# Kernel optimization log

Measured on AMD Instinct MI355X. Metric: run time of the kernel, lower is better.

## Reference

```python
import jax, jax.numpy as jnp
import numpy as np

L_LAYERS = 2
N = 128
T = 64
K_BANDS = 30
KMOD = K_BANDS + 2  # 32
B = 4
G4 = 4 * N
EPS = 1e-5


def setup_inputs() -> dict:
    key = jax.random.key(0)
    ks = iter(jax.random.split(key, 32))
    s = 1.0 / np.sqrt(N)

    def u(shape):
        return jax.random.uniform(next(ks), shape, jnp.float32, -s, s)

    inp = {"x": jax.random.normal(next(ks), (B, KMOD, T, N), jnp.float32)}
    # temporal modules: KMOD LSTM/fc instances per layer
    inp["tw_ih"] = u((L_LAYERS, KMOD, 2, G4, N))
    inp["tw_hh"] = u((L_LAYERS, KMOD, 2, G4, N))
    inp["tb_ih"] = u((L_LAYERS, KMOD, 2, G4))
    inp["tb_hh"] = u((L_LAYERS, KMOD, 2, G4))
    inp["tfc_w"] = u((L_LAYERS, KMOD, N, 2 * N))
    inp["tfc_b"] = u((L_LAYERS, KMOD, N))
    inp["tgn_g"] = jnp.ones((L_LAYERS, N), jnp.float32)
    inp["tgn_b"] = jnp.zeros((L_LAYERS, N), jnp.float32)
    # band modules: T LSTM/fc instances per layer
    inp["bw_ih"] = u((L_LAYERS, T, 2, G4, N))
    inp["bw_hh"] = u((L_LAYERS, T, 2, G4, N))
    inp["bb_ih"] = u((L_LAYERS, T, 2, G4))
    inp["bb_hh"] = u((L_LAYERS, T, 2, G4))
    inp["bfc_w"] = u((L_LAYERS, T, N, 2 * N))
    inp["bfc_b"] = u((L_LAYERS, T, N))
    inp["bgn_g"] = jnp.ones((L_LAYERS, N), jnp.float32)
    inp["bgn_b"] = jnp.zeros((L_LAYERS, N), jnp.float32)
    return inp


def groupnorm(X, gamma, beta):
    # GroupNorm(1, N) on [B, N, K, T] == normalize over all non-batch dims,
    # per-channel affine on the last (N) dim of the [B, K, T, N] layout.
    mu = X.mean(axis=(1, 2, 3), keepdims=True)
    var = X.var(axis=(1, 2, 3), keepdims=True)
    return (X - mu) * jax.lax.rsqrt(var + EPS) * gamma + beta


def bilstm(x, w_ih, w_hh, b_ih, b_hh):
    # x: [B, S, N]; w_ih/w_hh: [2, 4N, N]; biases: [2, 4N]. PyTorch gate order i,f,g,o.
    Bb, S, n = x.shape

    def run(xs, wih, whh, b):
        pre = jnp.einsum('bsn,gn->bsg', xs, wih) + b  # [B, S, 4N]

        def step(carry, p):
            h, c = carry
            g = p + h @ whh.T
            i, f, gg, o = jnp.split(g, 4, axis=-1)
            c = jax.nn.sigmoid(f) * c + jax.nn.sigmoid(i) * jnp.tanh(gg)
            h = jax.nn.sigmoid(o) * jnp.tanh(c)
            return (h, c), h

        z = jnp.zeros((Bb, n), xs.dtype)
        _, hs = jax.lax.scan(step, (z, z), jnp.swapaxes(pre, 0, 1))
        return jnp.swapaxes(hs, 0, 1)  # [B, S, N]

    fwd = run(x, w_ih[0], w_hh[0], b_ih[0] + b_hh[0])
    bwd = run(x[:, ::-1], w_ih[1], w_hh[1], b_ih[1] + b_hh[1])[:, ::-1]
    return jnp.concatenate([fwd, bwd], axis=-1)  # [B, S, 2N]


# vmap over the per-instance (band or frame) leading axis of inputs and weights
vbilstm = jax.vmap(bilstm, in_axes=(0, 0, 0, 0, 0))


def temporal_module(X, w_ih, w_hh, b_ih, b_hh, fc_w, fc_b, g, b):
    skip = X  # [B, K, T, N]
    Xn = groupnorm(X, g, b)
    xs = jnp.swapaxes(Xn, 0, 1)  # [K, B, T, N]
    h = vbilstm(xs, w_ih, w_hh, b_ih, b_hh)  # [K, B, T, 2N]
    out = jnp.einsum('kbtd,knd->kbtn', h, fc_w) + fc_b[:, None, None, :]
    return jnp.swapaxes(out, 0, 1) + skip


def band_module(X, w_ih, w_hh, b_ih, b_hh, fc_w, fc_b, g, b):
    skip = X  # [B, K, T, N]
    Xn = groupnorm(X, g, b)
    xs = jnp.transpose(Xn, (2, 0, 1, 3))  # [T, B, K, N]
    h = vbilstm(xs, w_ih, w_hh, b_ih, b_hh)  # [T, B, K, 2N]
    out = jnp.einsum('tbkd,tnd->tbkn', h, fc_w) + fc_b[:, None, None, :]
    return jnp.transpose(out, (1, 2, 0, 3)) + skip


def reference(x, tw_ih, tw_hh, tb_ih, tb_hh, tfc_w, tfc_b, tgn_g, tgn_b,
              bw_ih, bw_hh, bb_ih, bb_hh, bfc_w, bfc_b, bgn_g, bgn_b):
    X = x
    for i in range(L_LAYERS):
        X = temporal_module(X, tw_ih[i], tw_hh[i], tb_ih[i], tb_hh[i],
                            tfc_w[i], tfc_b[i], tgn_g[i], tgn_b[i])
        X = band_module(X, bw_ih[i], bw_hh[i], bb_ih[i], bb_hh[i],
                        bfc_w[i], bfc_b[i], bgn_g[i], bgn_b[i])
    return X[:, :K_BANDS, :, :]
```

## Files before the change

kernel.cpp:

```cpp
#include <hip/hip_runtime.h>
#include <hip/hip_bf16.h>
#include <cstddef>

#define BB 4
#define KK 32
#define TTT 64
#define NNC 128
#define GG4 512

__device__ __forceinline__ float sigm(float x) { return 1.f / (1.f + __expf(-x)); }
__device__ __forceinline__ float tanh_fast(float x) {
    x = fminf(fmaxf(x, -15.f), 15.f);
    float e = __expf(2.f * x);
    return (e - 1.f) / (e + 1.f);
}

__global__ void k_copy_red(const float4* __restrict__ src, float4* __restrict__ dst,
                           float* __restrict__ red2) {
    const int i = blockIdx.x * 256 + threadIdx.x;
    const float4 v = src[i];
    dst[i] = v;
    float s  = v.x + v.y + v.z + v.w;
    float ss = v.x * v.x + v.y * v.y + v.z * v.z + v.w * v.w;
    for (int off = 32; off; off >>= 1) {
        s  += __shfl_down(s, off);
        ss += __shfl_down(ss, off);
    }
    __shared__ float l0[4], l1[4];
    const int w = threadIdx.x >> 6;
    if ((threadIdx.x & 63) == 0) { l0[w] = s; l1[w] = ss; }
    __syncthreads();
    if (threadIdx.x == 0) {
        const int b = blockIdx.x >> 8, slot = blockIdx.x & 255;
        red2[(b * 256 + slot) * 2]     = l0[0] + l0[1] + l0[2] + l0[3];
        red2[(b * 256 + slot) * 2 + 1] = l1[0] + l1[1] + l1[2] + l1[3];
    }
}

template <bool BAND>
__global__ __launch_bounds__(1024, 1) void k_pre(
    const float* __restrict__ X, float* __restrict__ pre,
    const float* __restrict__ red2,
    const float* __restrict__ w_ih,
    const float* __restrict__ b_ih, const float* __restrict__ b_hh,
    const float* __restrict__ gn_g, const float* __restrict__ gn_b,
    int layer)
{
    constexpr int S    = BAND ? 32 : 64;
    constexpr int INST = BAND ? 64 : 32;
    const int tid = threadIdx.x;
    const int g   = tid & 511;
    const int hh  = tid >> 9;
    const int bid = blockIdx.x;
    const int b = bid & 3, dir = (bid >> 2) & 1, inst = bid >> 3;

    __shared__ float xn[S * 128];
    __shared__ float ex[4][1024];
    __shared__ float biasl[512];

    float s0 = 0.f, s1 = 0.f;
    {
        const float* rp = red2 + b * 512;
#pragma unroll 8
        for (int i = 0; i < 512; i += 2) { s0 += rp[i]; s1 += rp[i + 1]; }
    }
    const float mu = s0 * (1.0f / 262144.0f);
    const float rs = rsqrtf(fmaxf(s1 * (1.0f / 262144.0f) - mu * mu, 0.f) + 1e-5f);

    const size_t wbase = ((size_t)layer * INST + inst) * 2 + dir;
    if (tid < 512) biasl[tid] = b_ih[wbase * 512 + tid] + b_hh[wbase * 512 + tid];

    {
        const size_t xbase = BAND ? ((size_t)b * 2048 + inst) * 128
                                  : ((size_t)b * 32 + inst) * 64 * 128;
        const float* gmg = gn_g + layer * 128;
        const float* gmb = gn_b + layer * 128;
        for (int i4 = tid; i4 < S * 32; i4 += 1024) {
            int srow = i4 >> 5, n4 = i4 & 31;
            const float4 v = *(const float4*)(X + xbase +
                              (BAND ? (size_t)srow * 8192 : (size_t)srow * 128) + n4 * 4);
            const float4 ga = *(const float4*)(gmg + n4 * 4);
            const float4 be = *(const float4*)(gmb + n4 * 4);
            float4 o;
            o.x = (v.x - mu) * rs * ga.x + be.x;
            o.y = (v.y - mu) * rs * ga.y + be.y;
            o.z = (v.z - mu) * rs * ga.z + be.z;
            o.w = (v.w - mu) * rs * ga.w + be.w;
            *(float4*)(xn + srow * 128 + n4 * 4) = o;
        }
    }

    float4 w4[16];
    {
        const float* wr = w_ih + (wbase * 512 + g) * 128 + hh * 64;
#pragma unroll
        for (int j = 0; j < 16; ++j) w4[j] = *(const float4*)(wr + 4 * j);
    }
    __syncthreads();

    float* pb = pre + (size_t)bid * (S * 512);
    for (int st0 = 0; st0 < S; st0 += 4) {
#pragma unroll
        for (int q = 0; q < 4; ++q) {
            const int st = st0 + q;
            const int sidx = dir ? (S - 1 - st) : st;
            const float* xr = xn + sidx * 128 + hh * 64;
            float a0 = 0.f, a1 = 0.f, a2 = 0.f, a3 = 0.f;
#pragma unroll
            for (int j = 0; j < 4; ++j) {
                float4 hv0 = *(const float4*)(xr + 16 * j);
                float4 hv1 = *(const float4*)(xr + 16 * j + 4);
                float4 hv2 = *(const float4*)(xr + 16 * j + 8);
                float4 hv3 = *(const float4*)(xr + 16 * j + 12);
                a0 += w4[4*j].x   * hv0.x + w4[4*j].y   * hv0.y + w4[4*j].z   * hv0.z + w4[4*j].w   * hv0.w;
                a1 += w4[4*j+1].x * hv1.x + w4[4*j+1].y * hv1.y + w4[4*j+1].z * hv1.z + w4[4*j+1].w * hv1.w;
                a2 += w4[4*j+2].x * hv2.x + w4[4*j+2].y * hv2.y + w4[4*j+2].z * hv2.z + w4[4*j+2].w * hv2.w;
                a3 += w4[4*j+3].x * hv3.x + w4[4*j+3].y * hv3.y + w4[4*j+3].z * hv3.z + w4[4*j+3].w * hv3.w;
            }
            ex[q][hh * 512 + g] = (a0 + a1) + (a2 + a3);
        }
        __syncthreads();
        for (int idx = tid; idx < 4 * 512; idx += 1024) {
            const int q = idx >> 9, gg = idx & 511;
            const int u = gg & 127, gt = gg >> 7;
            pb[(size_t)(st0 + q) * 512 + u * 4 + gt] =
                ex[q][gg] + ex[q][512 + gg] + biasl[gg];
        }
        __syncthreads();
    }
}

template <bool BAND>
__global__ __launch_bounds__(1024, 1) void k_scan3(
    const float* __restrict__ pre, float* __restrict__ hout,
    const float* __restrict__ w_hh, int layer)
{
    constexpr int S    = BAND ? 32 : 64;
    constexpr int INST = BAND ? 64 : 32;
    constexpr int CH   = 8;
    constexpr int NCH  = S / CH;
    const int tid = threadIdx.x;
    const int u   = tid >> 3;
    const int j   = tid & 7;
    const int bid = blockIdx.x;
    const int b = bid & 3, dir = (bid >> 2) & 1, inst = bid >> 3;

    __shared__ float plds[2][CH * 512];
    __shared__ float hbuf[2][128];

    const size_t wbase = ((size_t)layer * INST + inst) * 2 + dir;
    float4 w4[4][4];
    {
        const float* wb = w_hh + wbase * 512 * 128;
#pragma unroll
        for (int gt = 0; gt < 4; ++gt) {
            const float* wr = wb + (size_t)(gt * 128 + u) * 128 + j * 16;
#pragma unroll
            for (int k = 0; k < 4; ++k) w4[gt][k] = *(const float4*)(wr + 4 * k);
        }
    }

    const float* pb = pre + (size_t)bid * (S * 512);
    ((float4*)plds[0])[tid] = ((const float4*)pb)[tid];
    if (tid < 256) ((float*)hbuf)[tid] = 0.f;
    __syncthreads();

    float c = 0.f;
    float* hob = hout + (((size_t)inst * 4 + b) * S) * 256 + dir * 128;

    int cur = 0;
    float4 pf;
    for (int ch = 0; ch < NCH; ++ch) {
        const int buf = ch & 1;
        if (ch + 1 < NCH)
            pf = ((const float4*)(pb + (size_t)(ch + 1) * CH * 512))[tid];
#pragma unroll
        for (int q = 0; q < CH; ++q) {
            const float* hr = &hbuf[cur][j * 16];
            const float4 hv0 = *(const float4*)(hr);
            const float4 hv1 = *(const float4*)(hr + 4);
            const float4 hv2 = *(const float4*)(hr + 8);
            const float4 hv3 = *(const float4*)(hr + 12);
            float acc0, acc1, acc2, acc3;
            {
                float a;
                a  = w4[0][0].x*hv0.x + w4[0][0].y*hv0.y + w4[0][0].z*hv0.z + w4[0][0].w*hv0.w;
                a += w4[0][1].x*hv1.x + w4[0][1].y*hv1.y + w4[0][1].z*hv1.z + w4[0][1].w*hv1.w;
                a += w4[0][2].x*hv2.x + w4[0][2].y*hv2.y + w4[0][2].z*hv2.z + w4[0][2].w*hv2.w;
                a += w4[0][3].x*hv3.x + w4[0][3].y*hv3.y + w4[0][3].z*hv3.z + w4[0][3].w*hv3.w;
                acc0 = a;
                a  = w4[1][0].x*hv0.x + w4[1][0].y*hv0.y + w4[1][0].z*hv0.z + w4[1][0].w*hv0.w;
                a += w4[1][1].x*hv1.x + w4[1][1].y*hv1.y + w4[1][1].z*hv1.z + w4[1][1].w*hv1.w;
                a += w4[1][2].x*hv2.x + w4[1][2].y*hv2.y + w4[1][2].z*hv2.z + w4[1][2].w*hv2.w;
                a += w4[1][3].x*hv3.x + w4[1][3].y*hv3.y + w4[1][3].z*hv3.z + w4[1][3].w*hv3.w;
                acc1 = a;
                a  = w4[2][0].x*hv0.x + w4[2][0].y*hv0.y + w4[2][0].z*hv0.z + w4[2][0].w*hv0.w;
                a += w4[2][1].x*hv1.x + w4[2][1].y*hv1.y + w4[2][1].z*hv1.z + w4[2][1].w*hv1.w;
                a += w4[2][2].x*hv2.x + w4[2][2].y*hv2.y + w4[2][2].z*hv2.z + w4[2][2].w*hv2.w;
                a += w4[2][3].x*hv3.x + w4[2][3].y*hv3.y + w4[2][3].z*hv3.z + w4[2][3].w*hv3.w;
                acc2 = a;
                a  = w4[3][0].x*hv0.x + w4[3][0].y*hv0.y + w4[3][0].z*hv0.z + w4[3][0].w*hv0.w;
                a += w4[3][1].x*hv1.x + w4[3][1].y*hv1.y + w4[3][1].z*hv1.z + w4[3][1].w*hv1.w;
                a += w4[3][2].x*hv2.x + w4[3][2].y*hv2.y + w4[3][2].z*hv2.z + w4[3][2].w*hv2.w;
                a += w4[3][3].x*hv3.x + w4[3][3].y*hv3.y + w4[3][3].z*hv3.z + w4[3][3].w*hv3.w;
                acc3 = a;
            }
#pragma unroll
            for (int off = 1; off < 8; off <<= 1) {
                acc0 += __shfl_xor(acc0, off);
                acc1 += __shfl_xor(acc1, off);
                acc2 += __shfl_xor(acc2, off);
                acc3 += __shfl_xor(acc3, off);
            }
            const float4 p4 = *(const float4*)&plds[buf][q * 512 + u * 4];
            const float gi = acc0 + p4.x;
            const float gf = acc1 + p4.y;
            const float gG = acc2 + p4.z;
            const float go = acc3 + p4.w;
            c = sigm(gf) * c + sigm(gi) * tanh_fast(gG);
            const float hval = sigm(go) * tanh_fast(c);
            const int nxt = cur ^ 1;
            if (j == 0) {
                hbuf[nxt][u] = hval;
                const int st = ch * CH + q;
                const int sidx = dir ? (S - 1 - st) : st;
                hob[(size_t)sidx * 256 + u] = hval;
            }
            if (q == CH - 1 && ch + 1 < NCH)
                ((float4*)plds[buf ^ 1])[tid] = pf;
            __syncthreads();
            cur = nxt;
        }
    }
}

template <bool BAND>
__global__ void k_fc(const float* __restrict__ h, const float* __restrict__ fc_w,
                     const float* __restrict__ fc_b, float* __restrict__ X,
                     float* __restrict__ red2, float* __restrict__ out,
                     int layer, int final_out)
{
    constexpr int S    = BAND ? 32 : 64;
    constexpr int INST = BAND ? 64 : 32;
    constexpr int RPB  = 8;
    constexpr int CPB  = S / RPB;
    const int inst  = blockIdx.x / (BB * CPB);
    const int chunk = blockIdx.x % (BB * CPB);

    __shared__ float hs[RPB * 256];
    const int tid = threadIdx.x;
    const float* hbase = h + ((size_t)inst * BB * S + chunk * RPB) * 256;
    for (int i = tid; i < RPB * 64; i += 256)
        ((float4*)hs)[i] = ((const float4*)hbase)[i];
    __syncthreads();

    const int n  = tid & 127;
    const int rg = tid >> 7;
    const float* wrow = fc_w + (((size_t)layer * INST + inst) * 128 + n) * 256;
    float4 a0 = {0,0,0,0}, a1 = {0,0,0,0}, a2 = {0,0,0,0}, a3 = {0,0,0,0};
#pragma unroll 8
    for (int d4 = 0; d4 < 64; ++d4) {
        float4 wv = ((const float4*)wrow)[d4];
        float4 h0 = ((const float4*)(hs + (rg * 4 + 0) * 256))[d4];
        float4 h1 = ((const float4*)(hs + (rg * 4 + 1) * 256))[d4];
        float4 h2 = ((const float4*)(hs + (rg * 4 + 2) * 256))[d4];
        float4 h3 = ((const float4*)(hs + (rg * 4 + 3) * 256))[d4];
        a0.x += wv.x*h0.x; a0.y += wv.y*h0.y; a0.z += wv.z*h0.z; a0.w += wv.w*h0.w;
        a1.x += wv.x*h1.x; a1.y += wv.y*h1.y; a1.z += wv.z*h1.z; a1.w += wv.w*h1.w;
        a2.x += wv.x*h2.x; a2.y += wv.y*h2.y; a2.z += wv.z*h2.z; a2.w += wv.w*h2.w;
        a3.x += wv.x*h3.x; a3.y += wv.y*h3.y; a3.z += wv.z*h3.z; a3.w += wv.w*h3.w;
    }
    const float bias = fc_b[((size_t)layer * INST + inst) * 128 + n];
    float acc[4];
    acc[0] = (a0.x + a0.y) + (a0.z + a0.w);
    acc[1] = (a1.x + a1.y) + (a1.z + a1.w);
    acc[2] = (a2.x + a2.y) + (a2.z + a2.w);
    acc[3] = (a3.x + a3.y) + (a3.z + a3.w);

    float s = 0.f, ss = 0.f;
#pragma unroll
    for (int i = 0; i < 4; ++i) {
        const int r = chunk * RPB + rg * 4 + i;
        const int b = r / S, sd = r % S;
        const size_t xi = BAND ? (((size_t)b * 32 + sd) * 64 + inst) * 128 + n
                               : (((size_t)b * 32 + inst) * 64 + sd) * 128 + n;
        const float v = X[xi] + acc[i] + bias;
        X[xi] = v;
        s += v; ss += v * v;
        if (BAND && final_out && sd < 30)
            out[(((size_t)b * 30 + sd) * 64 + inst) * 128 + n] = v;
    }
    for (int off = 32; off; off >>= 1) {
        s  += __shfl_down(s, off);
        ss += __shfl_down(ss, off);
    }
    __shared__ float l0[4], l1[4];
    const int w = tid >> 6;
    if ((tid & 63) == 0) { l0[w] = s; l1[w] = ss; }
    __syncthreads();
    if (tid == 0) {
        const int bsel = chunk / CPB;
        const int slot = inst * CPB + (chunk % CPB);
        red2[(bsel * 256 + slot) * 2]     = l0[0] + l0[1] + l0[2] + l0[3];
        red2[(bsel * 256 + slot) * 2 + 1] = l1[0] + l1[1] + l1[2] + l1[3];
    }
}

extern "C" void kernel_launch(void* const* d_in, const int* in_sizes, int n_in,
                              void* d_out, int out_size, void* d_ws, size_t ws_size,
                              hipStream_t stream) {
    const float* x     = (const float*)d_in[0];
    const float* tw_ih = (const float*)d_in[1];
    const float* tw_hh = (const float*)d_in[2];
    const float* tb_ih = (const float*)d_in[3];
    const float* tb_hh = (const float*)d_in[4];
    const float* tfc_w = (const float*)d_in[5];
    const float* tfc_b = (const float*)d_in[6];
    const float* tgn_g = (const float*)d_in[7];
    const float* tgn_b = (const float*)d_in[8];
    const float* bw_ih = (const float*)d_in[9];
    const float* bw_hh = (const float*)d_in[10];
    const float* bb_ih = (const float*)d_in[11];
    const float* bb_hh = (const float*)d_in[12];
    const float* bfc_w = (const float*)d_in[13];
    const float* bfc_b = (const float*)d_in[14];
    const float* bgn_g = (const float*)d_in[15];
    const float* bgn_b = (const float*)d_in[16];

    float* X    = (float*)d_ws;
    float* h    = X + 1048576;
    float* red2 = h + 2097152;
    float* pre  = red2 + 2048;
    float* out  = (float*)d_out;

    k_copy_red<<<1024, 256, 0, stream>>>((const float4*)x, (float4*)X, red2);

    for (int layer = 0; layer < 2; ++layer) {
        k_pre<false><<<256, 1024, 0, stream>>>(X, pre, red2, tw_ih, tb_ih, tb_hh,
                                               tgn_g, tgn_b, layer);
        k_scan3<false><<<256, 1024, 0, stream>>>(pre, h, tw_hh, layer);
        k_fc<false><<<1024, 256, 0, stream>>>(h, tfc_w, tfc_b, X, red2, out, layer, 0);
        k_pre<true><<<512, 1024, 0, stream>>>(X, pre, red2, bw_ih, bb_ih, bb_hh,
                                              bgn_g, bgn_b, layer);
        k_scan3<true><<<512, 1024, 0, stream>>>(pre, h, bw_hh, layer);
        k_fc<true><<<1024, 256, 0, stream>>>(h, bfc_w, bfc_b, X, red2, out,
                                             layer, layer == 1 ? 1 : 0);
    }
}
```

Measured before the change: 987.8 us.

## Assign one gate row per thread in input-projection and recurrent scan kernels

Both the input-projection and recurrent-scan kernels now use 512 threads per block, one thread per gate row, with the full 128-wide weight row held in registers. This removes the cross-thread shuffle and shared-memory reductions and the gate-interleaved pre layout. The scan now applies the gate activations in parallel across all 512 threads, then 128 threads update the cell state. The cost is 128 float registers of weights per thread, which risks spilling, plus a second barrier per time step in the scan.

```diff
diff --git a/kernel.cpp b/kernel.cpp
--- a/kernel.cpp
+++ b/kernel.cpp
@@ -37,8 +37,27 @@
     }
 }
 
+#define DOT32(WARR, XV4)                                                        \
+    {                                                                           \
+        _Pragma("unroll")                                                       \
+        for (int k = 0; k < 8; ++k) {                                           \
+            const float4 h0 = XV4[4 * k];                                       \
+            const float4 h1 = XV4[4 * k + 1];                                   \
+            const float4 h2 = XV4[4 * k + 2];                                   \
+            const float4 h3 = XV4[4 * k + 3];                                   \
+            a0 += WARR[4*k].x   * h0.x + WARR[4*k].y   * h0.y                   \
+                + WARR[4*k].z   * h0.z + WARR[4*k].w   * h0.w;                  \
+            a1 += WARR[4*k+1].x * h1.x + WARR[4*k+1].y * h1.y                   \
+                + WARR[4*k+1].z * h1.z + WARR[4*k+1].w * h1.w;                  \
+            a2 += WARR[4*k+2].x * h2.x + WARR[4*k+2].y * h2.y                   \
+                + WARR[4*k+2].z * h2.z + WARR[4*k+2].w * h2.w;                  \
+            a3 += WARR[4*k+3].x * h3.x + WARR[4*k+3].y * h3.y                   \
+                + WARR[4*k+3].z * h3.z + WARR[4*k+3].w * h3.w;                  \
+        }                                                                       \
+    }
+
 template <bool BAND>
-__global__ __launch_bounds__(1024, 1) void k_pre(
+__global__ __launch_bounds__(512, 2) void k_pre4(
     const float* __restrict__ X, float* __restrict__ pre,
     const float* __restrict__ red2,
     const float* __restrict__ w_ih,
@@ -48,15 +67,11 @@
 {
     constexpr int S    = BAND ? 32 : 64;
     constexpr int INST = BAND ? 64 : 32;
-    const int tid = threadIdx.x;
-    const int g   = tid & 511;
-    const int hh  = tid >> 9;
+    const int g   = threadIdx.x;
     const int bid = blockIdx.x;
     const int b = bid & 3, dir = (bid >> 2) & 1, inst = bid >> 3;
 
     __shared__ float xn[S * 128];
-    __shared__ float ex[4][1024];
-    __shared__ float biasl[512];
 
     float s0 = 0.f, s1 = 0.f;
     {
@@ -66,16 +81,13 @@
     }
     const float mu = s0 * (1.0f / 262144.0f);
     const float rs = rsqrtf(fmaxf(s1 * (1.0f / 262144.0f) - mu * mu, 0.f) + 1e-5f);
-
-    const size_t wbase = ((size_t)layer * INST + inst) * 2 + dir;
-    if (tid < 512) biasl[tid] = b_ih[wbase * 512 + tid] + b_hh[wbase * 512 + tid];
 
     {
         const size_t xbase = BAND ? ((size_t)b * 2048 + inst) * 128
                                   : ((size_t)b * 32 + inst) * 64 * 128;
         const float* gmg = gn_g + layer * 128;
         const float* gmb = gn_b + layer * 128;
-        for (int i4 = tid; i4 < S * 32; i4 += 1024) {
+        for (int i4 = g; i4 < S * 32; i4 += 512) {
             int srow = i4 >> 5, n4 = i4 & 31;
             const float4 v = *(const float4*)(X + xbase +
                               (BAND ? (size_t)srow * 8192 : (size_t)srow * 128) + n4 * 4);
@@ -90,147 +102,80 @@
         }
     }
 
-    float4 w4[16];
-    {
-        const float* wr = w_ih + (wbase * 512 + g) * 128 + hh * 64;
+    const size_t wbase = ((size_t)layer * INST + inst) * 2 + dir;
+    float4 w4[32];
+    {
+        const float* wr = w_ih + (wbase * 512 + g) * 128;
 #pragma unroll
-        for (int j = 0; j < 16; ++j) w4[j] = *(const float4*)(wr + 4 * j);
-    }
-    __syncthreads();
-
-    float* pb = pre + (size_t)bid * (S * 512);
-    for (int st0 = 0; st0 < S; st0 += 4) {
-#pragma unroll
-        for (int q = 0; q < 4; ++q) {
-            const int st = st0 + q;
-            const int sidx = dir ? (S - 1 - st) : st;
-            const float* xr = xn + sidx * 128 + hh * 64;
-            float a0 = 0.f, a1 = 0.f, a2 = 0.f, a3 = 0.f;
-#pragma unroll
-            for (int j = 0; j < 4; ++j) {
-                float4 hv0 = *(const float4*)(xr + 16 * j);
-                float4 hv1 = *(const float4*)(xr + 16 * j + 4);
-                float4 hv2 = *(const float4*)(xr + 16 * j + 8);
-                float4 hv3 = *(const float4*)(xr + 16 * j + 12);
-                a0 += w4[4*j].x   * hv0.x + w4[4*j].y   * hv0.y + w4[4*j].z   * hv0.z + w4[4*j].w   * hv0.w;
-                a1 += w4[4*j+1].x * hv1.x + w4[4*j+1].y * hv1.y + w4[4*j+1].z * hv1.z + w4[4*j+1].w * hv1.w;
-                a2 += w4[4*j+2].x * hv2.x + w4[4*j+2].y * hv2.y + w4[4*j+2].z * hv2.z + w4[4*j+2].w * hv2.w;
-                a3 += w4[4*j+3].x * hv3.x + w4[4*j+3].y * hv3.y + w4[4*j+3].z * hv3.z + w4[4*j+3].w * hv3.w;
-            }
-            ex[q][hh * 512 + g] = (a0 + a1) + (a2 + a3);
-        }
-        __syncthreads();
-        for (int idx = tid; idx < 4 * 512; idx += 1024) {
-            const int q = idx >> 9, gg = idx & 511;
-            const int u = gg & 127, gt = gg >> 7;
-            pb[(size_t)(st0 + q) * 512 + u * 4 + gt] =
-                ex[q][gg] + ex[q][512 + gg] + biasl[gg];
-        }
-        __syncthreads();
+        for (int k = 0; k < 32; ++k) w4[k] = *(const float4*)(wr + 4 * k);
+    }
+    const float bias = b_ih[wbase * 512 + g] + b_hh[wbase * 512 + g];
+    __syncthreads();
+
+    float* pb = pre + (size_t)bid * (S * 512) + g;
+    for (int st = 0; st < S; ++st) {
+        const int sidx = dir ? (S - 1 - st) : st;
+        const float4* xr = (const float4*)(xn + sidx * 128);
+        float a0 = bias, a1 = 0.f, a2 = 0.f, a3 = 0.f;
+        DOT32(w4, xr)
+        pb[(size_t)st * 512] = (a0 + a1) + (a2 + a3);
     }
 }
 
 template <bool BAND>
-__global__ __launch_bounds__(1024, 1) void k_scan3(
+__global__ __launch_bounds__(512, 2) void k_scan4(
     const float* __restrict__ pre, float* __restrict__ hout,
     const float* __restrict__ w_hh, int layer)
 {
     constexpr int S    = BAND ? 32 : 64;
     constexpr int INST = BAND ? 64 : 32;
-    constexpr int CH   = 8;
-    constexpr int NCH  = S / CH;
-    const int tid = threadIdx.x;
-    const int u   = tid >> 3;
-    const int j   = tid & 7;
+    const int g   = threadIdx.x;
     const int bid = blockIdx.x;
     const int b = bid & 3, dir = (bid >> 2) & 1, inst = bid >> 3;
 
-    __shared__ float plds[2][CH * 512];
+    __shared__ float gbuf[512];
     __shared__ float hbuf[2][128];
 
     const size_t wbase = ((size_t)layer * INST + inst) * 2 + dir;
-    float4 w4[4][4];
-    {
-        const float* wb = w_hh + wbase * 512 * 128;
+    float4 w4[32];
+    {
+        const float* wr = w_hh + (wbase * 512 + g) * 128;
 #pragma unroll
-        for (int gt = 0; gt < 4; ++gt) {
-            const float* wr = wb + (size_t)(gt * 128 + u) * 128 + j * 16;
-#pragma unroll
-            for (int k = 0; k < 4; ++k) w4[gt][k] = *(const float4*)(wr + 4 * k);
+        for (int k = 0; k < 32; ++k) w4[k] = *(const float4*)(wr + 4 * k);
+    }
+
+    const float* pb = pre + (size_t)bid * (S * 512) + g;
+    float pcur = pb[0];
+    if (g < 128) { hbuf[0][g] = 0.f; hbuf[1][g] = 0.f; }
+    float c = 0.f;
+    __syncthreads();
+
+    float* hob = hout + (((size_t)inst * 4 + b) * S) * 256 + dir * 128;
+    int cur = 0;
+
+    for (int st = 0; st < S; ++st) {
+        const float pnext = (st + 1 < S) ? pb[(size_t)(st + 1) * 512] : 0.f;
+        const float4* hv4 = (const float4*)hbuf[cur];
+        float a0 = pcur, a1 = 0.f, a2 = 0.f, a3 = 0.f;
+        DOT32(w4, hv4)
+        const float dot = (a0 + a1) + (a2 + a3);
+        const float act = ((g >> 7) == 2) ? tanh_fast(dot) : sigm(dot);
+        gbuf[g] = act;
+        __syncthreads();
+        if (g < 128) {
+            const float gi = gbuf[g];
+            const float gf = gbuf[g + 128];
+            const float gG = gbuf[g + 256];
+            const float go = gbuf[g + 384];
+            c = gf * c + gi * gG;
+            const float hval = go * tanh_fast(c);
+            hbuf[cur ^ 1][g] = hval;
+            const int sidx = dir ? (S - 1 - st) : st;
+            hob[(size_t)sidx * 256 + g] = hval;
         }
-    }
-
-    const float* pb = pre + (size_t)bid * (S * 512);
-    ((float4*)plds[0])[tid] = ((const float4*)pb)[tid];
-    if (tid < 256) ((float*)hbuf)[tid] = 0.f;
-    __syncthreads();
-
-    float c = 0.f;
-    float* hob = hout + (((size_t)inst * 4 + b) * S) * 256 + dir * 128;
-
-    int cur = 0;
-    float4 pf;
-    for (int ch = 0; ch < NCH; ++ch) {
-        const int buf = ch & 1;
-        if (ch + 1 < NCH)
-            pf = ((const float4*)(pb + (size_t)(ch + 1) * CH * 512))[tid];
-#pragma unroll
-        for (int q = 0; q < CH; ++q) {
-            const float* hr = &hbuf[cur][j * 16];
-            const float4 hv0 = *(const float4*)(hr);
-            const float4 hv1 = *(const float4*)(hr + 4);
-            const float4 hv2 = *(const float4*)(hr + 8);
-            const float4 hv3 = *(const float4*)(hr + 12);
-            float acc0, acc1, acc2, acc3;
-            {
-                float a;
-                a  = w4[0][0].x*hv0.x + w4[0][0].y*hv0.y + w4[0][0].z*hv0.z + w4[0][0].w*hv0.w;
-                a += w4[0][1].x*hv1.x + w4[0][1].y*hv1.y + w4[0][1].z*hv1.z + w4[0][1].w*hv1.w;
-                a += w4[0][2].x*hv2.x + w4[0][2].y*hv2.y + w4[0][2].z*hv2.z + w4[0][2].w*hv2.w;
-                a += w4[0][3].x*hv3.x + w4[0][3].y*hv3.y + w4[0][3].z*hv3.z + w4[0][3].w*hv3.w;
-                acc0 = a;
-                a  = w4[1][0].x*hv0.x + w4[1][0].y*hv0.y + w4[1][0].z*hv0.z + w4[1][0].w*hv0.w;
-                a += w4[1][1].x*hv1.x + w4[1][1].y*hv1.y + w4[1][1].z*hv1.z + w4[1][1].w*hv1.w;
-                a += w4[1][2].x*hv2.x + w4[1][2].y*hv2.y + w4[1][2].z*hv2.z + w4[1][2].w*hv2.w;
-                a += w4[1][3].x*hv3.x + w4[1][3].y*hv3.y + w4[1][3].z*hv3.z + w4[1][3].w*hv3.w;
-                acc1 = a;
-                a  = w4[2][0].x*hv0.x + w4[2][0].y*hv0.y + w4[2][0].z*hv0.z + w4[2][0].w*hv0.w;
-                a += w4[2][1].x*hv1.x + w4[2][1].y*hv1.y + w4[2][1].z*hv1.z + w4[2][1].w*hv1.w;
-                a += w4[2][2].x*hv2.x + w4[2][2].y*hv2.y + w4[2][2].z*hv2.z + w4[2][2].w*hv2.w;
-                a += w4[2][3].x*hv3.x + w4[2][3].y*hv3.y + w4[2][3].z*hv3.z + w4[2][3].w*hv3.w;
-                acc2 = a;
-                a  = w4[3][0].x*hv0.x + w4[3][0].y*hv0.y + w4[3][0].z*hv0.z + w4[3][0].w*hv0.w;
-                a += w4[3][1].x*hv1.x + w4[3][1].y*hv1.y + w4[3][1].z*hv1.z + w4[3][1].w*hv1.w;
-                a += w4[3][2].x*hv2.x + w4[3][2].y*hv2.y + w4[3][2].z*hv2.z + w4[3][2].w*hv2.w;
-                a += w4[3][3].x*hv3.x + w4[3][3].y*hv3.y + w4[3][3].z*hv3.z + w4[3][3].w*hv3.w;
-                acc3 = a;
-            }
-#pragma unroll
-            for (int off = 1; off < 8; off <<= 1) {
-                acc0 += __shfl_xor(acc0, off);
-                acc1 += __shfl_xor(acc1, off);
-                acc2 += __shfl_xor(acc2, off);
-                acc3 += __shfl_xor(acc3, off);
-            }
-            const float4 p4 = *(const float4*)&plds[buf][q * 512 + u * 4];
-            const float gi = acc0 + p4.x;
-            const float gf = acc1 + p4.y;
-            const float gG = acc2 + p4.z;
-            const float go = acc3 + p4.w;
-            c = sigm(gf) * c + sigm(gi) * tanh_fast(gG);
-            const float hval = sigm(go) * tanh_fast(c);
-            const int nxt = cur ^ 1;
-            if (j == 0) {
-                hbuf[nxt][u] = hval;
-                const int st = ch * CH + q;
-                const int sidx = dir ? (S - 1 - st) : st;
-                hob[(size_t)sidx * 256 + u] = hval;
-            }
-            if (q == CH - 1 && ch + 1 < NCH)
-                ((float4*)plds[buf ^ 1])[tid] = pf;
-            __syncthreads();
-            cur = nxt;
-        }
+        __syncthreads();
+        pcur = pnext;
+        cur ^= 1;
     }
 }
 
@@ -336,13 +281,13 @@
     k_copy_red<<<1024, 256, 0, stream>>>((const float4*)x, (float4*)X, red2);
 
     for (int layer = 0; layer < 2; ++layer) {
-        k_pre<false><<<256, 1024, 0, stream>>>(X, pre, red2, tw_ih, tb_ih, tb_hh,
+        k_pre4<false><<<256, 512, 0, stream>>>(X, pre, red2, tw_ih, tb_ih, tb_hh,
                                                tgn_g, tgn_b, layer);
-        k_scan3<false><<<256, 1024, 0, stream>>>(pre, h, tw_hh, layer);
+        k_scan4<false><<<256, 512, 0, stream>>>(pre, h, tw_hh, layer);
         k_fc<false><<<1024, 256, 0, stream>>>(h, tfc_w, tfc_b, X, red2, out, layer, 0);
-        k_pre<true><<<512, 1024, 0, stream>>>(X, pre, red2, bw_ih, bb_ih, bb_hh,
+        k_pre4<true><<<512, 512, 0, stream>>>(X, pre, red2, bw_ih, bb_ih, bb_hh,
                                               bgn_g, bgn_b, layer);
-        k_scan3<true><<<512, 1024, 0, stream>>>(pre, h, bw_hh, layer);
+        k_scan4<true><<<512, 512, 0, stream>>>(pre, h, bw_hh, layer);
         k_fc<true><<<1024, 256, 0, stream>>>(h, bfc_w, bfc_b, X, red2, out,
                                              layer, layer == 1 ? 1 : 0);
     }
```

Result: slower. 1.650 ms (+67.1%).
